# Kernel tuning notes

Measured on AMD Instinct MI355X. Metric: run time of the kernel, lower is better.

Reference implementation:

```python
import jax, jax.numpy as jnp
import numpy as np
from jax import lax

B, C, H, W = 32, 256, 56, 56

def _conv(x, w, stride, groups=1, pad='VALID'):
    return lax.conv_general_dilated(x, w, (stride, stride), pad,
                                    feature_group_count=groups,
                                    dimension_numbers=('NCHW', 'OIHW', 'NCHW'))

def _ln(x, g, b, eps=1e-5):
    mu = jnp.mean(x, -1, keepdims=True)
    var = jnp.mean((x - mu) ** 2, -1, keepdims=True)
    return (x - mu) * lax.rsqrt(var + eps) * g + b

def setup_inputs() -> dict:
    key = jax.random.key(0)
    ks = jax.random.split(key, 16)
    s = 0.02
    Ch = C // 2
    d = {}
    d['x'] = jax.random.normal(ks[0], (B, C, H, W), jnp.float32)
    d['Wq'] = jax.random.normal(ks[1], (C, C), jnp.float32) * s;  d['bq'] = jnp.zeros((C,), jnp.float32)
    d['Wk'] = jax.random.normal(ks[2], (C, C), jnp.float32) * s;  d['bk'] = jnp.zeros((C,), jnp.float32)
    d['Wv'] = jax.random.normal(ks[3], (C, C), jnp.float32) * s;  d['bv'] = jnp.zeros((C,), jnp.float32)
    d['sr1_w'] = jax.random.normal(ks[4], (C, C, 8, 8), jnp.float32) * s; d['sr1_b'] = jnp.zeros((C,), jnp.float32)
    d['ln1_g'] = jnp.ones((C,), jnp.float32); d['ln1_b'] = jnp.zeros((C,), jnp.float32)
    d['sr2_w'] = jax.random.normal(ks[5], (C, C, 4, 4), jnp.float32) * s; d['sr2_b'] = jnp.zeros((C,), jnp.float32)
    d['ln2_g'] = jnp.ones((C,), jnp.float32); d['ln2_b'] = jnp.zeros((C,), jnp.float32)
    d['Wkv1'] = jax.random.normal(ks[6], (C, C), jnp.float32) * s; d['bkv1'] = jnp.zeros((C,), jnp.float32)
    d['Wkv2'] = jax.random.normal(ks[7], (C, C), jnp.float32) * s; d['bkv2'] = jnp.zeros((C,), jnp.float32)
    d['lc1_w'] = jax.random.normal(ks[8], (Ch, 1, 3, 3), jnp.float32) * s; d['lc1_b'] = jnp.zeros((Ch,), jnp.float32)
    d['lc2_w'] = jax.random.normal(ks[9], (Ch, 1, 3, 3), jnp.float32) * s; d['lc2_b'] = jnp.zeros((Ch,), jnp.float32)
    d['rp_w'] = jax.random.normal(ks[10], (C, C), jnp.float32) * s;  d['rp_b'] = jnp.zeros((C,), jnp.float32)
    d['rp12_w'] = jax.random.normal(ks[11], (C, C), jnp.float32) * s; d['rp12_b'] = jnp.zeros((C,), jnp.float32)
    d['dw_w'] = jax.random.normal(ks[12], (C, 2), jnp.float32) * 0.5  # Conv3d (2,1,1) depthwise, no bias
    return d

def reference(x, Wq, bq, Wk, bk, Wv, bv, sr1_w, sr1_b, ln1_g, ln1_b,
              sr2_w, sr2_b, ln2_g, ln2_b, Wkv1, bkv1, Wkv2, bkv2,
              lc1_w, lc1_b, lc2_w, lc2_b, rp_w, rp_b, rp12_w, rp12_b, dw_w):
    Bx, Cc, h, w = x.shape
    N = h * w
    Ch = Cc // 2
    xt = x.reshape(Bx, Cc, N).transpose(0, 2, 1)                 # [B,N,C]
    q = jax.nn.softmax(xt @ Wq + bq, axis=-1)                    # softmax over channels
    q1, q2 = q[..., :Ch], q[..., Ch:]

    # spatial-reduction branches (conv -> LN -> GELU)
    x1 = _conv(x, sr1_w, 8) + sr1_b[:, None, None]               # [B,C,7,7]
    x1 = jax.nn.gelu(_ln(x1.reshape(Bx, Cc, -1).transpose(0, 2, 1), ln1_g, ln1_b), approximate=False)
    x2 = _conv(x, sr2_w, 4) + sr2_b[:, None, None]               # [B,C,14,14]
    x2 = jax.nn.gelu(_ln(x2.reshape(Bx, Cc, -1).transpose(0, 2, 1), ln2_g, ln2_b), approximate=False)

    def branch(xr, Wkv, bkv, lc_w, lc_b, qh, hh):
        kv = (xr @ Wkv + bkv).reshape(Bx, -1, 2, Ch)
        k = jax.nn.softmax(kv[:, :, 0], axis=1)                  # softmax over reduced tokens
        v = kv[:, :, 1]
        vsp = v.transpose(0, 2, 1).reshape(Bx, Ch, hh, hh)
        v = v + (_conv(vsp, lc_w, 1, groups=Ch, pad='SAME') + lc_b[:, None, None]).reshape(Bx, Ch, -1).transpose(0, 2, 1)
        ctx = jnp.einsum('bnk,bnv->bkv', k, v)                   # [B,Ch,Ch]
        return jnp.einsum('bnk,bkv->bnv', qh, ctx)               # [B,N,Ch]

    a1 = branch(x1, Wkv1, bkv1, lc1_w, lc1_b, q1, 7)
    a2 = branch(x2, Wkv2, bkv2, lc2_w, lc2_b, q2, 14)
    eff2 = jnp.concatenate([a1, a2], axis=-1)                    # [B,N,C]
    eff2 = jnp.einsum('bni,oi->bon', eff2, rp12_w).reshape(Bx, Cc, h, w) + rp12_b[None, :, None, None]

    # global efficient-attention branch
    keys = jax.nn.softmax(xt @ Wk + bk, axis=1)                  # softmax over tokens
    values = xt @ Wv + bv
    ctx = jnp.einsum('bnk,bnv->bkv', keys, values)               # [B,C,C]
    att = jnp.einsum('bnk,bkv->bnv', q, ctx)                     # [B,N,C]
    eff = jnp.einsum('bni,oi->bon', att, rp_w).reshape(Bx, Cc, h, w) + rp_b[None, :, None, None]

    # Conv3d (2,1,1) depthwise merge over the two branches
    out = eff * dw_w[:, 0][None, :, None, None] + eff2 * dw_w[:, 1][None, :, None, None]
    return out
```

## Files before the change

kernel.cpp:

```cpp
#include <hip/hip_runtime.h>
#include <hip/hip_bf16.h>
#include <math.h>

#define B_ 32
#define H_ 56
#define W_ 56
#define N_ 3136
#define NT_ 100352

typedef short short8 __attribute__((ext_vector_type(8)));
typedef float f32x4 __attribute__((ext_vector_type(4)));

__device__ __forceinline__ unsigned short f2b(float f){
  union { float f; unsigned u; } v; v.f = f;
  return (unsigned short)((v.u + 0x7FFFu + ((v.u>>16)&1u)) >> 16);
}

#define LDSW(row, bo) ((unsigned)((row)*128 + ((bo) ^ (((row)&7)<<4))))

__device__ __forceinline__ short8 ldfrag(const char* base, int row, int kk){
  return *(const short8*)(base + LDSW(row, kk*2));
}
__device__ __forceinline__ f32x4 mfma16(short8 a, short8 b, f32x4 c){
  return __builtin_amdgcn_mfma_f32_16x16x32_bf16(a, b, c, 0, 0, 0);
}
__device__ __forceinline__ void gld16(void* lds, const void* g){
  __builtin_amdgcn_global_load_lds((__attribute__((address_space(1))) void*)g,
                                   (__attribute__((address_space(3))) void*)lds,
                                   16, 0, 0);
}

__global__ void prep_trans_kernel(
    const float* __restrict__ x, unsigned short* __restrict__ xt,
    const float* __restrict__ Wq, const float* __restrict__ Wk,
    const float* __restrict__ Wv, const float* __restrict__ Wkv1,
    const float* __restrict__ Wkv2, const float* __restrict__ sr1w,
    const float* __restrict__ sr2w, const float* __restrict__ rpw,
    const float* __restrict__ rpb, const float* __restrict__ rp12w,
    const float* __restrict__ rp12b, const float* __restrict__ dww,
    unsigned short* WqT, unsigned short* WkT, unsigned short* WvT,
    unsigned short* Wkv1T, unsigned short* Wkv2T,
    unsigned short* srw1, unsigned short* srw2,
    unsigned short* Acomb, float* bias_out)
{
  __shared__ float tile[64][65];
  if (blockIdx.x < 6272){
    int bn = blockIdx.x >> 2; int b = bn / 49; int n0 = (bn - b*49)*64;
    int c0 = (blockIdx.x & 3)*64;
    int t = threadIdx.x;
    {
      int cl = t >> 2, nq = t & 3;
      const float* src = x + ((size_t)(b*256 + c0 + cl))*N_ + n0 + nq*16;
#pragma unroll
      for (int j = 0; j < 4; j++){
        float4 v = *(const float4*)(src + j*4);
        tile[cl][nq*16 + j*4 + 0] = v.x;
        tile[cl][nq*16 + j*4 + 1] = v.y;
        tile[cl][nq*16 + j*4 + 2] = v.z;
        tile[cl][nq*16 + j*4 + 3] = v.w;
      }
    }
    __syncthreads();
    {
      int nl = t >> 2, cq = t & 3;
      unsigned short pk[16];
#pragma unroll
      for (int j=0;j<16;j++) pk[j] = f2b(tile[cq*16+j][nl]);
      unsigned short* dst = xt + ((size_t)(b*N_ + n0 + nl))*256 + c0 + cq*16;
      *(uint4*)dst = *(uint4*)&pk[0];
      *(uint4*)(dst+8) = *(uint4*)&pk[8];
    }
    return;
  }
  int idx = (blockIdx.x - 6272)*256 + threadIdx.x;
  const int stride = 2048*256;
  const int total = 5*65536 + 4194304 + 1048576 + 131072 + 256;
  for (int i = idx; i < total; i += stride) {
    int j = i;
    if (j < 5*65536) {
      int w = j >> 16, e = j & 65535;
      int o = e >> 8, c = e & 255;
      const float* src = (w==0)?Wq:(w==1)?Wk:(w==2)?Wv:(w==3)?Wkv1:Wkv2;
      unsigned short* dst = (w==0)?WqT:(w==1)?WkT:(w==2)?WvT:(w==3)?Wkv1T:Wkv2T;
      dst[o*256+c] = f2b(src[c*256+o]);
      continue;
    }
    j -= 5*65536;
    if (j < 4194304) {
      int o = j >> 14, rem = j & 16383, pos = rem >> 8, c = rem & 255;
      srw1[j] = f2b(sr1w[o*16384 + c*64 + pos]);
      continue;
    }
    j -= 4194304;
    if (j < 1048576) {
      int o = j >> 12, rem = j & 4095, pos = rem >> 8, c = rem & 255;
      srw2[j] = f2b(sr2w[o*4096 + c*16 + pos]);
      continue;
    }
    j -= 1048576;
    if (j < 131072) {
      int o = j >> 9, i2 = j & 511;
      float v = (i2 < 256) ? dww[o*2+0]*rpw[o*256+i2]
                           : dww[o*2+1]*rp12w[o*256+(i2-256)];
      Acomb[o*512+i2] = f2b(v);
      continue;
    }
    j -= 131072;
    bias_out[j] = dww[j*2+0]*rpb[j] + dww[j*2+1]*rp12b[j];
  }
}

__global__ __launch_bounds__(256,2) void qkv3_kernel(
    const unsigned short* __restrict__ xt,
    const unsigned short* __restrict__ WqT, const unsigned short* __restrict__ WkT,
    const unsigned short* __restrict__ WvT,
    const float* __restrict__ bq, const float* __restrict__ bk, const float* __restrict__ bv,
    unsigned short* __restrict__ qbuf, unsigned short* __restrict__ KexpT,
    unsigned short* __restrict__ VT, float* __restrict__ s_q, float* __restrict__ s_k)
{
  __shared__ __align__(16) char smem[32768 + 32768 + 1024];
  char* At = smem;
  char* Bt = smem + 32768;
  float* redbuf = (float*)(smem + 65536);
  const int t = threadIdx.x, wave = t>>6, lane = t&63, l15 = lane&15, l4 = lane>>4;
  const int r0 = blockIdx.x*64;
  const int b = r0 / N_;
  const int nl0 = r0 - b*N_;

#pragma unroll
  for (int c4=0;c4<4;c4++)
#pragma unroll
    for (int j=0;j<2;j++){
      int chunk = j*256 + t; int row = chunk>>3, c8 = chunk&7;
      int c8s = c8 ^ (row&7);
      gld16(At + c4*8192 + (j*256 + wave*64)*16,
            xt + (size_t)(r0+row)*256 + c4*64 + c8s*8);
    }
  __syncthreads();

  for (int mat=0; mat<3; mat++){
    const unsigned short* BT = (mat==0)?WqT:(mat==1)?WkT:WvT;
    const float* bias = (mat==0)?bq:(mat==1)?bk:bv;
    const f32x4 vzero = {0.f,0.f,0.f,0.f};
    f32x4 acc[4][4];
#pragma unroll
    for (int i=0;i<4;i++)
#pragma unroll
      for (int j=0;j<4;j++) acc[i][j] = vzero;

    for (int k0c=0;k0c<4;k0c++){
#pragma unroll
      for (int j=0;j<8;j++){
        int chunk = j*256 + t; int row = chunk>>3, c8 = chunk&7;
        int c8s = c8 ^ (row&7);
        gld16(Bt + (j*256 + wave*64)*16, BT + (size_t)row*256 + k0c*64 + c8s*8);
      }
      __syncthreads();
#pragma unroll
      for (int ks=0;ks<2;ks++){
        short8 af[4], bfr[4];
#pragma unroll
        for (int mi=0;mi<4;mi++) af[mi]  = ldfrag(At + k0c*8192, mi*16 + l15, ks*32 + l4*8);
#pragma unroll
        for (int ni=0;ni<4;ni++) bfr[ni] = ldfrag(Bt, wave*64 + ni*16 + l15, ks*32 + l4*8);
#pragma unroll
        for (int mi=0;mi<4;mi++)
#pragma unroll
          for (int ni=0;ni<4;ni++)
            acc[mi][ni] = mfma16(af[mi], bfr[ni], acc[mi][ni]);
      }
      __syncthreads();
    }

    float bb4[4];
#pragma unroll
    for (int ni=0;ni<4;ni++) bb4[ni] = bias[wave*64 + ni*16 + l15];

    if (mat == 0) {
      float rs[4][4];
#pragma unroll
      for (int mi=0;mi<4;mi++)
#pragma unroll
        for (int r=0;r<4;r++) rs[mi][r] = 0.f;
#pragma unroll
      for (int mi=0;mi<4;mi++)
#pragma unroll
        for (int ni=0;ni<4;ni++)
#pragma unroll
          for (int r=0;r<4;r++){
            float e = __expf(acc[mi][ni][r] + bb4[ni]);
            acc[mi][ni][r] = e;
            rs[mi][r] += e;
          }
#pragma unroll
      for (int mi=0;mi<4;mi++)
#pragma unroll
        for (int r=0;r<4;r++){
          float s = rs[mi][r];
          s += __shfl_xor(s, 1); s += __shfl_xor(s, 2);
          s += __shfl_xor(s, 4); s += __shfl_xor(s, 8);
          rs[mi][r] = s;
        }
      if (l15 == 0){
#pragma unroll
        for (int mi=0;mi<4;mi++)
#pragma unroll
          for (int r=0;r<4;r++)
            redbuf[wave*64 + mi*16 + l4*4 + r] = rs[mi][r];
      }
      __syncthreads();
      unsigned short* qb = (unsigned short*)Bt;
#pragma unroll
      for (int mi=0;mi<4;mi++)
#pragma unroll
        for (int r=0;r<4;r++){
          int rr = mi*16 + l4*4 + r;
#pragma unroll
          for (int ni=0;ni<4;ni++)
            qb[rr*256 + wave*64 + ni*16 + l15] = f2b(acc[mi][ni][r]);
        }
      if (t < 64){
        s_q[r0 + t] = redbuf[t] + redbuf[64+t] + redbuf[128+t] + redbuf[192+t];
      }
      __syncthreads();
#pragma unroll
      for (int j=0;j<8;j++){
        int chunk = j*256 + t;
        int row = chunk >> 5, c8 = chunk & 31;
        *(uint4*)(qbuf + (size_t)(r0+row)*256 + c8*8) = *(const uint4*)(qb + row*256 + c8*8);
      }
      __syncthreads();
    } else {
      float cs[4] = {0.f,0.f,0.f,0.f};
#pragma unroll
      for (int mi=0;mi<4;mi++)
#pragma unroll
        for (int ni=0;ni<4;ni++)
#pragma unroll
          for (int r=0;r<4;r++){
            float v = acc[mi][ni][r] + bb4[ni];
            if (mat == 1){ v = __expf(v); cs[ni] += v; }
            int row = mi*16 + l4*4 + r;
            int col = wave*64 + ni*16 + l15;
            *(unsigned short*)(Bt + LDSW(col, row*2)) = f2b(v);
          }
      if (mat == 1){
#pragma unroll
        for (int ni=0;ni<4;ni++){
          float s = cs[ni];
          s += __shfl_xor(s, 16);
          s += __shfl_xor(s, 32);
          if (lane < 16) atomicAdd(&s_k[b*256 + wave*64 + ni*16 + lane], s);
        }
      }
      __syncthreads();
      unsigned short* ot = (mat==1) ? KexpT : VT;
#pragma unroll
      for (int j=0;j<8;j++){
        int chunk = j*256 + t;
        int c = chunk >> 3, n8 = chunk & 7;
        *(uint4*)(ot + ((size_t)b*256 + c)*N_ + nl0 + n8*8) = *(const uint4*)(Bt + LDSW(c, n8*16));
      }
      __syncthreads();
    }
  }
}

template<int S, int OW, int KW, int NSK, int MPB, int KTOT>
__device__ __forceinline__ void srconv_body(
    const unsigned short* __restrict__ xt, const unsigned short* __restrict__ wbf,
    float* __restrict__ part, int bid, char* At, char* Bt)
{
  const int KCH = KTOT / NSK;
  const int Mtot = B_*MPB;
  const int sk = bid % NSK, tile = bid / NSK;
  const int t = threadIdx.x, wave = t>>6, lane = t&63, l15 = lane&15, l4 = lane>>4;
  const f32x4 vzero = {0.f,0.f,0.f,0.f};
  f32x4 acc[4][4];
#pragma unroll
  for (int i=0;i<4;i++)
#pragma unroll
    for (int j=0;j<4;j++) acc[i][j] = vzero;

  size_t abase[2];
#pragma unroll
  for (int j=0;j<2;j++){
    int chunk = j*256 + t;
    int row = chunk >> 3, c8 = chunk & 7;
    int c8s = c8 ^ (row&7);
    int rowc = tile*64 + row; if (rowc > Mtot-1) rowc = Mtot-1;
    int b = rowc / MPB; int m = rowc - b*MPB;
    int p = m / OW; int q = m - p*OW;
    abase[j] = ((size_t)b*N_ + (size_t)(S*p)*W_ + S*q)*256 + c8s*8;
  }

  for (int kt = 0; kt < KCH; kt += 64){
    const int k0 = sk*KCH + kt;
    const int pos = k0 >> 8, cc = k0 & 255;
    const int dy = pos / KW, dx = pos - dy*KW;
    const size_t off = (size_t)(dy*W_ + dx)*256 + cc;
#pragma unroll
    for (int j=0;j<2;j++){
      gld16(At + (j*256 + wave*64)*16, xt + abase[j] + off);
    }
#pragma unroll
    for (int j=0;j<8;j++){
      int chunk = j*256 + t; int row = chunk>>3, c8 = chunk&7;
      int c8s = c8 ^ (row&7);
      gld16(Bt + (j*256 + wave*64)*16, wbf + (size_t)row*KTOT + k0 + c8s*8);
    }
    __syncthreads();
#pragma unroll
    for (int ks=0;ks<2;ks++){
      short8 af[4], bfr[4];
#pragma unroll
      for (int mi=0;mi<4;mi++) af[mi]  = ldfrag(At, mi*16 + l15, ks*32 + l4*8);
#pragma unroll
      for (int ni=0;ni<4;ni++) bfr[ni] = ldfrag(Bt, wave*64 + ni*16 + l15, ks*32 + l4*8);
#pragma unroll
      for (int mi=0;mi<4;mi++)
#pragma unroll
        for (int ni=0;ni<4;ni++)
          acc[mi][ni] = mfma16(af[mi], bfr[ni], acc[mi][ni]);
    }
    __syncthreads();
  }
#pragma unroll
  for (int mi=0;mi<4;mi++)
#pragma unroll
    for (int r=0;r<4;r++){
      int row = tile*64 + mi*16 + l4*4 + r;
      if (row < Mtot){
        size_t basep = ((size_t)sk*Mtot + row)*256;
#pragma unroll
        for (int ni=0;ni<4;ni++)
          part[basep + wave*64 + ni*16 + l15] = acc[mi][ni][r];
      }
    }
}

__device__ __forceinline__ void ctxmain_body(
    const unsigned short* __restrict__ KexpT, const unsigned short* __restrict__ VT,
    float* __restrict__ part, int orig, char* At, char* Bt)
{
  const int idx = (orig & 7)*112 + (orig >> 3);
  const int b = idx / 28; int rem = idx - b*28;
  const int sk = rem >> 2, y = rem & 3;
  const int mt = y >> 1, nt = y & 1;
  const int it0 = sk*7, it1 = it0+7;
  const int t = threadIdx.x;
  const int wave = t>>6, lane = t&63, l15 = lane&15, l4 = lane>>4;
  const int wm = (wave>>1)*64, wn = (wave&1)*64;
  const unsigned short* A  = KexpT + ((size_t)b*256 + mt*128)*N_;
  const unsigned short* Bv = VT + ((size_t)b*256 + nt*128)*N_;
  const f32x4 vzero = {0.f,0.f,0.f,0.f};
  f32x4 acc[4][4];
#pragma unroll
  for (int i=0;i<4;i++)
#pragma unroll
    for (int j=0;j<4;j++) acc[i][j] = vzero;

  for (int it=it0; it<it1; it++){
    const int k0 = it*64;
#pragma unroll
    for (int j=0;j<4;j++){
      int chunk = j*256 + t; int row = chunk>>3, c8 = chunk&7;
      int c8s = c8 ^ (row&7);
      gld16(At + (j*256 + wave*64)*16, A + (size_t)row*N_ + k0 + c8s*8);
    }
#pragma unroll
    for (int j=0;j<4;j++){
      int chunk = j*256 + t; int row = chunk>>3, c8 = chunk&7;
      int c8s = c8 ^ (row&7);
      gld16(Bt + (j*256 + wave*64)*16, Bv + (size_t)row*N_ + k0 + c8s*8);
    }
    __syncthreads();
#pragma unroll
    for (int ks=0;ks<2;ks++){
      short8 af[4], bfr[4];
#pragma unroll
      for (int mi=0;mi<4;mi++) af[mi]  = ldfrag(At, wm + mi*16 + l15, ks*32 + l4*8);
#pragma unroll
      for (int ni=0;ni<4;ni++) bfr[ni] = ldfrag(Bt, wn + ni*16 + l15, ks*32 + l4*8);
#pragma unroll
      for (int mi=0;mi<4;mi++)
#pragma unroll
        for (int ni=0;ni<4;ni++)
          acc[mi][ni] = mfma16(af[mi], bfr[ni], acc[mi][ni]);
    }
    __syncthreads();
  }
#pragma unroll
  for (int mi=0;mi<4;mi++)
#pragma unroll
    for (int r=0;r<4;r++){
      int kg = mt*128 + wm + mi*16 + l4*4 + r;
      size_t basep = (((size_t)sk*B_ + b)*256 + kg)*256 + nt*128 + wn;
#pragma unroll
      for (int ni=0;ni<4;ni++)
        part[basep + ni*16 + l15] = acc[mi][ni][r];
    }
}

__global__ __launch_bounds__(256,4) void conv_ctx_kernel(
    const unsigned short* __restrict__ xt, const unsigned short* __restrict__ srw1,
    const unsigned short* __restrict__ srw2, float* __restrict__ x1part,
    float* __restrict__ x2part, const unsigned short* __restrict__ KexpT,
    const unsigned short* __restrict__ VT, float* __restrict__ ctxpart)
{
  __shared__ __align__(16) char smem[8192 + 32768];
  if (blockIdx.x < 392)
    srconv_body<4,14,4,4,196,4096>(xt, srw2, x2part, blockIdx.x, smem, smem+8192);
  else if (blockIdx.x < 792)
    srconv_body<8,7,8,16,49,16384>(xt, srw1, x1part, blockIdx.x-392, smem, smem+8192);
  else
    ctxmain_body(KexpT, VT, ctxpart, blockIdx.x-792, smem, smem+16384);
}

__device__ __forceinline__ void lngelu_body(
    const float* __restrict__ part, const float* __restrict__ srb,
    const float* __restrict__ g, const float* __restrict__ bb,
    unsigned short* __restrict__ out, int M, int nsk, int Mtot, int bid,
    float* red)
{
  int b = bid / M, m = bid - b*M;
  int c = threadIdx.x;
  float v = srb[c];
  for (int s=0;s<nsk;s++) v += part[((size_t)s*Mtot + b*M + m)*256 + c];
  int wave = c>>6, lane = c&63;
  float s1 = v;
  s1 += __shfl_xor(s1,1); s1 += __shfl_xor(s1,2); s1 += __shfl_xor(s1,4);
  s1 += __shfl_xor(s1,8); s1 += __shfl_xor(s1,16); s1 += __shfl_xor(s1,32);
  if (lane==0) red[wave] = s1;
  __syncthreads();
  float mu = (red[0]+red[1]+red[2]+red[3]) * (1.0f/256.0f);
  float d = v - mu;
  float s2 = d*d;
  s2 += __shfl_xor(s2,1); s2 += __shfl_xor(s2,2); s2 += __shfl_xor(s2,4);
  s2 += __shfl_xor(s2,8); s2 += __shfl_xor(s2,16); s2 += __shfl_xor(s2,32);
  if (lane==0) red[4+wave] = s2;
  __syncthreads();
  float var = (red[4]+red[5]+red[6]+red[7]) * (1.0f/256.0f);
  float y = d * rsqrtf(var + 1e-5f) * g[c] + bb[c];
  float ge = 0.5f * y * (1.0f + erff(y * 0.70710678118654752f));
  out[((size_t)b*M + m)*256 + c] = f2b(ge);
}

__global__ __launch_bounds__(256) void red_ln_kernel(
    const float* __restrict__ x1part, const float* __restrict__ x2part,
    const float* __restrict__ sr1b, const float* __restrict__ sr2b,
    const float* __restrict__ ln1g, const float* __restrict__ ln1b,
    const float* __restrict__ ln2g, const float* __restrict__ ln2b,
    unsigned short* __restrict__ x1g, unsigned short* __restrict__ x2g,
    const float* __restrict__ ctxpart, const float* __restrict__ s_k,
    unsigned short* __restrict__ ctxcomb)
{
  __shared__ float red[8];
  if (blockIdx.x < 1568){
    lngelu_body(x1part, sr1b, ln1g, ln1b, x1g, 49, 16, 1568, blockIdx.x, red);
  } else if (blockIdx.x < 7840){
    lngelu_body(x2part, sr2b, ln2g, ln2b, x2g, 196, 4, 6272, blockIdx.x-1568, red);
  } else {
    int e = ((blockIdx.x-7840)*256 + threadIdx.x)*4;
    int b = e >> 16; int rem = e & 65535; int kg = rem >> 8; int col = rem & 255;
    float4 s = {0.f,0.f,0.f,0.f};
#pragma unroll
    for (int sk=0; sk<7; sk++){
      float4 p = *(const float4*)(ctxpart + ((((size_t)sk*B_ + b)*256 + kg)<<8) + col);
      s.x += p.x; s.y += p.y; s.z += p.z; s.w += p.w;
    }
    float inv = 1.0f / s_k[b*256 + kg];
    unsigned short pk[4] = {f2b(s.x*inv), f2b(s.y*inv), f2b(s.z*inv), f2b(s.w*inv)};
    *(uint2*)(ctxcomb + ((size_t)b*256 + kg)*512 + col) = *(uint2*)&pk[0];
  }
}

__global__ __launch_bounds__(256,2) void gmat_kernel(
    const unsigned short* __restrict__ Acomb, const unsigned short* __restrict__ ctxcomb,
    unsigned short* __restrict__ outg)
{
  __shared__ __align__(16) char smem[32768];
  char* At = smem; char* Bt = smem + 16384;
  const int b = blockIdx.x, mt = blockIdx.y, nt = blockIdx.z;
  const int t = threadIdx.x;
  const int wave = t>>6, lane = t&63, l15 = lane&15, l4 = lane>>4;
  const int wm = (wave>>1)*64, wn = (wave&1)*64;
  const unsigned short* A  = Acomb + (size_t)mt*128*512;
  const unsigned short* Bv = ctxcomb + ((size_t)b*256 + nt*128)*512;
  const f32x4 vzero = {0.f,0.f,0.f,0.f};
  f32x4 acc[4][4];
#pragma unroll
  for (int i=0;i<4;i++)
#pragma unroll
    for (int j=0;j<4;j++) acc[i][j] = vzero;

  for (int it=0; it<8; it++){
    const int k0 = it*64;
#pragma unroll
    for (int j=0;j<4;j++){
      int chunk = j*256 + t; int row = chunk>>3, c8 = chunk&7;
      int c8s = c8 ^ (row&7);
      gld16(At + (j*256 + wave*64)*16, A + (size_t)row*512 + k0 + c8s*8);
    }
#pragma unroll
    for (int j=0;j<4;j++){
      int chunk = j*256 + t; int row = chunk>>3, c8 = chunk&7;
      int c8s = c8 ^ (row&7);
      gld16(Bt + (j*256 + wave*64)*16, Bv + (size_t)row*512 + k0 + c8s*8);
    }
    __syncthreads();
#pragma unroll
    for (int ks=0;ks<2;ks++){
      short8 af[4], bfr[4];
#pragma unroll
      for (int mi=0;mi<4;mi++) af[mi]  = ldfrag(At, wm + mi*16 + l15, ks*32 + l4*8);
#pragma unroll
      for (int ni=0;ni<4;ni++) bfr[ni] = ldfrag(Bt, wn + ni*16 + l15, ks*32 + l4*8);
#pragma unroll
      for (int mi=0;mi<4;mi++)
#pragma unroll
        for (int ni=0;ni<4;ni++)
          acc[mi][ni] = mfma16(af[mi], bfr[ni], acc[mi][ni]);
    }
    __syncthreads();
  }
#pragma unroll
  for (int mi=0;mi<4;mi++)
#pragma unroll
    for (int r=0;r<4;r++){
      int og = mt*128 + wm + mi*16 + l4*4 + r;
#pragma unroll
      for (int ni=0;ni<4;ni++)
        outg[(size_t)b*65536 + (size_t)og*256 + nt*128 + wn + ni*16 + l15] = f2b(acc[mi][ni][r]);
    }
}

__global__ __launch_bounds__(256,4) void kv_both_kernel(
    const unsigned short* __restrict__ x1g, const unsigned short* __restrict__ Wkv1T,
    const float* __restrict__ bkv1, float* __restrict__ kexp1, float* __restrict__ vraw1,
    const unsigned short* __restrict__ x2g, const unsigned short* __restrict__ Wkv2T,
    const float* __restrict__ bkv2, float* __restrict__ kexp2, float* __restrict__ vraw2)
{
  __shared__ __align__(16) char smem[8192 + 16384];
  char* At = smem; char* Bt = smem + 8192;
  const int half = blockIdx.x & 1;
  int bid = blockIdx.x >> 1;
  const unsigned short* A; const unsigned short* BT; const float* bias;
  float* kexp; float* vraw; int r0; int R;
  if (bid < 25){ A=x1g; BT=Wkv1T; bias=bkv1; kexp=kexp1; vraw=vraw1; r0=bid*64; R=1568; }
  else { A=x2g; BT=Wkv2T; bias=bkv2; kexp=kexp2; vraw=vraw2; r0=(bid-25)*64; R=6272; }
  const int t = threadIdx.x, wave = t>>6, lane = t&63, l15 = lane&15, l4 = lane>>4;
  const int wn = wave*32;
  const f32x4 vzero = {0.f,0.f,0.f,0.f};
  f32x4 acc[4][2];
#pragma unroll
  for (int i=0;i<4;i++){ acc[i][0] = vzero; acc[i][1] = vzero; }

  for (int k0 = 0; k0 < 256; k0 += 64) {
#pragma unroll
    for (int j = 0; j < 2; j++){
      int chunk = j*256 + t;
      int row = chunk >> 3, c8 = chunk & 7;
      int c8s = c8 ^ (row&7);
      int rg = r0 + row; if (rg > R-1) rg = R-1;
      gld16(At + (j*256 + wave*64)*16, A + (size_t)rg*256 + k0 + c8s*8);
    }
#pragma unroll
    for (int j = 0; j < 4; j++){
      int chunk = j*256 + t;
      int row = chunk >> 3, c8 = chunk & 7;
      int c8s = c8 ^ (row&7);
      gld16(Bt + (j*256 + wave*64)*16, BT + (size_t)(half*128 + row)*256 + k0 + c8s*8);
    }
    __syncthreads();
#pragma unroll
    for (int ks = 0; ks < 2; ks++){
      short8 af[4], bfr[2];
#pragma unroll
      for (int mi=0;mi<4;mi++) af[mi]  = ldfrag(At, mi*16 + l15, ks*32 + l4*8);
#pragma unroll
      for (int ni=0;ni<2;ni++) bfr[ni] = ldfrag(Bt, wn + ni*16 + l15, ks*32 + l4*8);
#pragma unroll
      for (int mi=0;mi<4;mi++)
#pragma unroll
        for (int ni=0;ni<2;ni++)
          acc[mi][ni] = mfma16(af[mi], bfr[ni], acc[mi][ni]);
    }
    __syncthreads();
  }
  float bb2[2];
#pragma unroll
  for (int ni=0;ni<2;ni++) bb2[ni] = bias[half*128 + wn + ni*16 + l15];
#pragma unroll
  for (int mi=0;mi<4;mi++)
#pragma unroll
    for (int ni=0;ni<2;ni++)
#pragma unroll
      for (int r=0;r<4;r++){
        int rg = r0 + mi*16 + l4*4 + r;
        if (rg < R){
          int col = wn + ni*16 + l15;
          float v = acc[mi][ni][r] + bb2[ni];
          if (half == 0) kexp[(size_t)rg*128 + col] = __expf(v);
          else           vraw[(size_t)rg*128 + col] = v;
        }
      }
}

__device__ __forceinline__ void dwconv_body(
    const float* __restrict__ vraw, const float* __restrict__ lcw,
    const float* __restrict__ lcb, float* __restrict__ vmod, int M, int OW, int idx)
{
  int ch = idx & 127; int rest = idx >> 7; int m = rest % M; int b = rest / M;
  if (b >= B_) return;
  int py = m / OW, px = m - py*OW;
  float acc = vraw[((size_t)b*M + m)*128 + ch] + lcb[ch];
#pragma unroll
  for (int dy=0;dy<3;dy++)
#pragma unroll
    for (int dx=0;dx<3;dx++){
      int yy = py+dy-1, xx = px+dx-1;
      if (yy>=0 && yy<OW && xx>=0 && xx<OW)
        acc += vraw[((size_t)b*M + yy*OW+xx)*128 + ch] * lcw[ch*9 + dy*3 + dx];
    }
  vmod[((size_t)b*M + m)*128 + ch] = acc;
}

__global__ __launch_bounds__(256) void dwconv_both_kernel(
    const float* __restrict__ vraw1, const float* __restrict__ lc1w,
    const float* __restrict__ lc1b, float* __restrict__ vmod1,
    const float* __restrict__ vraw2, const float* __restrict__ lc2w,
    const float* __restrict__ lc2b, float* __restrict__ vmod2)
{
  int gid = blockIdx.x*256 + threadIdx.x;
  if (blockIdx.x < 784) dwconv_body(vraw1, lc1w, lc1b, vmod1, 49, 7, gid);
  else dwconv_body(vraw2, lc2w, lc2b, vmod2, 196, 14, gid - 784*256);
}

__global__ __launch_bounds__(512) void ctxbr_both_kernel(
    const float* __restrict__ kexp1, const float* __restrict__ vmod1,
    const float* __restrict__ kexp2, const float* __restrict__ vmod2,
    unsigned short* __restrict__ ctxcomb)
{
  const int b = blockIdx.x;
  int kc = blockIdx.y;
  const float* kexp; const float* vmod; int M, BR;
  if (kc < 32){ kexp = kexp1; vmod = vmod1; M = 49; BR = 0; }
  else { kexp = kexp2; vmod = vmod2; M = 196; BR = 1; kc -= 32; }
  const int t = threadIdx.x;
  const int kl = t >> 7, j = t & 127;
  const int kk = kc*4 + kl;
  const float* kp = kexp + (size_t)b*M*128 + kk;
  const float* vp = vmod + (size_t)b*M*128 + j;
  float acc = 0.f, s = 0.f;
  for (int m = 0; m < M; m++){
    float kv = kp[(size_t)m*128];
    s += kv;
    acc += kv * vp[(size_t)m*128];
  }
  const int krow = BR ? (128+kk) : kk;
  unsigned short* dst = ctxcomb + ((size_t)b*256 + krow)*512;
  const int wbase = BR ? 384 : 256;
  const int zbase = BR ? 256 : 384;
  dst[wbase + j] = f2b(acc / s);
  dst[zbase + j] = 0;
}

__global__ __launch_bounds__(256,4) void final_kernel(
    const unsigned short* __restrict__ Gmat, const unsigned short* __restrict__ qbuf,
    const float* __restrict__ bias_out, const float* __restrict__ s_q,
    float* __restrict__ out)
{
  __shared__ __align__(16) char smem[16384 + 8192];
  char* At = smem; char* Bt = smem + 16384;
  const int b = blockIdx.x, ot = blockIdx.y, nt = blockIdx.z;
  const int t = threadIdx.x, wave = t>>6, lane = t&63, l15 = lane&15, l4 = lane>>4;
  const int wm = (wave>>1)*64, wn = (wave&1)*32;
  const unsigned short* A  = Gmat + ((size_t)b*256 + ot*128)*256;
  const unsigned short* Bq = qbuf + ((size_t)b*N_ + nt*64)*256;
  const f32x4 vzero = {0.f,0.f,0.f,0.f};
  f32x4 acc[4][2];
#pragma unroll
  for (int i=0;i<4;i++){ acc[i][0] = vzero; acc[i][1] = vzero; }

  for (int k0=0;k0<256;k0+=64){
#pragma unroll
    for (int j=0;j<4;j++){
      int chunk = j*256 + t; int row = chunk>>3, c8 = chunk&7;
      int c8s = c8 ^ (row&7);
      gld16(At + (j*256 + wave*64)*16, A + (size_t)row*256 + k0 + c8s*8);
    }
#pragma unroll
    for (int j=0;j<2;j++){
      int chunk = j*256 + t; int row = chunk>>3, c8 = chunk&7;
      int c8s = c8 ^ (row&7);
      gld16(Bt + (j*256 + wave*64)*16, Bq + (size_t)row*256 + k0 + c8s*8);
    }
    __syncthreads();
#pragma unroll
    for (int ks=0;ks<2;ks++){
      short8 af[4], bfr[2];
#pragma unroll
      for (int mi=0;mi<4;mi++) af[mi]  = ldfrag(At, wm + mi*16 + l15, ks*32 + l4*8);
#pragma unroll
      for (int ni=0;ni<2;ni++) bfr[ni] = ldfrag(Bt, wn + ni*16 + l15, ks*32 + l4*8);
#pragma unroll
      for (int mi=0;mi<4;mi++)
#pragma unroll
        for (int ni=0;ni<2;ni++)
          acc[mi][ni] = mfma16(af[mi], bfr[ni], acc[mi][ni]);
    }
    __syncthreads();
  }
  float iq[2];
#pragma unroll
  for (int ni=0;ni<2;ni++)
    iq[ni] = 1.0f / s_q[(size_t)b*N_ + nt*64 + wn + ni*16 + l15];
#pragma unroll
  for (int mi=0;mi<4;mi++)
#pragma unroll
    for (int r=0;r<4;r++){
      int o = ot*128 + wm + mi*16 + l4*4 + r;
      float bo = bias_out[o];
#pragma unroll
      for (int ni=0;ni<2;ni++){
        int n = nt*64 + wn + ni*16 + l15;
        out[((size_t)b*256 + o)*N_ + n] = acc[mi][ni][r]*iq[ni] + bo;
      }
    }
}

extern "C" void kernel_launch(void* const* d_in, const int* in_sizes, int n_in,
                              void* d_out, int out_size, void* d_ws, size_t ws_size,
                              hipStream_t stream)
{
  const float* x     = (const float*)d_in[0];
  const float* Wq    = (const float*)d_in[1];
  const float* bq    = (const float*)d_in[2];
  const float* Wk    = (const float*)d_in[3];
  const float* bk    = (const float*)d_in[4];
  const float* Wv    = (const float*)d_in[5];
  const float* bv    = (const float*)d_in[6];
  const float* sr1w  = (const float*)d_in[7];
  const float* sr1b  = (const float*)d_in[8];
  const float* ln1g  = (const float*)d_in[9];
  const float* ln1b  = (const float*)d_in[10];
  const float* sr2w  = (const float*)d_in[11];
  const float* sr2b  = (const float*)d_in[12];
  const float* ln2g  = (const float*)d_in[13];
  const float* ln2b  = (const float*)d_in[14];
  const float* Wkv1  = (const float*)d_in[15];
  const float* bkv1  = (const float*)d_in[16];
  const float* Wkv2  = (const float*)d_in[17];
  const float* bkv2  = (const float*)d_in[18];
  const float* lc1w  = (const float*)d_in[19];
  const float* lc1b  = (const float*)d_in[20];
  const float* lc2w  = (const float*)d_in[21];
  const float* lc2b  = (const float*)d_in[22];
  const float* rpw   = (const float*)d_in[23];
  const float* rpb   = (const float*)d_in[24];
  const float* rp12w = (const float*)d_in[25];
  const float* rp12b = (const float*)d_in[26];
  const float* dww   = (const float*)d_in[27];

  char* ws = (char*)d_ws;
  size_t off = 0;
  auto take = [&](size_t n)->char*{ char* p = ws + off; off += (n + 255) & ~(size_t)255; return p; };

  unsigned short* WqT   = (unsigned short*)take(131072);
  unsigned short* WkT   = (unsigned short*)take(131072);
  unsigned short* WvT   = (unsigned short*)take(131072);
  unsigned short* Wkv1T = (unsigned short*)take(131072);
  unsigned short* Wkv2T = (unsigned short*)take(131072);
  unsigned short* srw1  = (unsigned short*)take(8388608);
  unsigned short* srw2  = (unsigned short*)take(2097152);
  unsigned short* Acomb = (unsigned short*)take(262144);
  float* bias_out = (float*)take(1024);
  float* s_k      = (float*)take(32768);
  float* s_q      = (float*)take(401408);
  char* regionA = take(51380224);
  unsigned short* qbuf = (unsigned short*)take(51380224);
  char* regionK = take(51380224);
  char* regionV = take(51380224);
  float* x1part = (float*)take(25690112);
  if (off > ws_size) return;

  unsigned short* xt    = (unsigned short*)regionA;
  unsigned short* KexpT = (unsigned short*)regionK;
  unsigned short* VT = (unsigned short*)regionV;
  unsigned short* Gmat = (unsigned short*)regionV;
  unsigned short* x1g  = (unsigned short*)(regionV + 4194304);
  unsigned short* x2g  = (unsigned short*)(regionV + 4997120);
  float* kexp1 = (float*)(regionV + 8208384);
  float* vraw1 = (float*)(regionV + 9011200);
  float* vmod1 = (float*)(regionV + 9814016);
  float* kexp2 = (float*)(regionV + 10616832);
  float* vraw2 = (float*)(regionV + 13828096);
  float* vmod2 = (float*)(regionV + 17039360);
  unsigned short* ctxcomb = (unsigned short*)d_out;
  float* ctxpart = (float*)((char*)d_out + 8388608);
  float* x2part  = (float*)((char*)d_out + 67108864);

  hipMemsetAsync(s_k, 0, 32768, stream);
  prep_trans_kernel<<<8320, 256, 0, stream>>>(x, xt,
                                              Wq, Wk, Wv, Wkv1, Wkv2, sr1w, sr2w,
                                              rpw, rpb, rp12w, rp12b, dww,
                                              WqT, WkT, WvT, Wkv1T, Wkv2T, srw1, srw2,
                                              Acomb, bias_out);
  qkv3_kernel<<<1568, 256, 0, stream>>>(xt, WqT, WkT, WvT, bq, bk, bv,
                                        qbuf, KexpT, VT, s_q, s_k);
  conv_ctx_kernel<<<392+400+896, 256, 0, stream>>>(xt, srw1, srw2,
                                                   x1part, x2part, KexpT, VT, ctxpart);
  red_ln_kernel<<<7840+2048, 256, 0, stream>>>(x1part, x2part, sr1b, sr2b,
                                               ln1g, ln1b, ln2g, ln2b, x1g, x2g,
                                               ctxpart, s_k, ctxcomb);
  kv_both_kernel<<<246, 256, 0, stream>>>(x1g, Wkv1T, bkv1, kexp1, vraw1,
                                          x2g, Wkv2T, bkv2, kexp2, vraw2);
  dwconv_both_kernel<<<3920, 256, 0, stream>>>(vraw1, lc1w, lc1b, vmod1,
                                               vraw2, lc2w, lc2b, vmod2);
  ctxbr_both_kernel<<<dim3(32,64), 512, 0, stream>>>(kexp1, vmod1, kexp2, vmod2, ctxcomb);
  gmat_kernel<<<dim3(32,2,2), 256, 0, stream>>>(Acomb, ctxcomb, Gmat);
  final_kernel<<<dim3(32,2,49), 256, 0, stream>>>(Gmat, qbuf, bias_out, s_q, (float*)d_out);
}
```

Measured before the change: 400.9 us.

## Co-schedule spatial-reduction convs with QKV projection and split out context GEMM

The strided spatial-reduction convolutions move out of the context kernel and into the QKV projection launch, interleaved two QKV blocks to one conv block by block index. The context GEMM becomes its own kernel. Both convs and the QKV GEMM read only xt, so they can overlap on the GPU instead of the convs waiting for QKV to finish. The trade-offs are that the conv blocks now run under the QKV kernel's larger shared-memory footprint and 256x2 launch bounds, which may lower their occupancy, and that the separate context kernel adds one launch.

```diff
diff --git a/kernel.cpp b/kernel.cpp
--- a/kernel.cpp
+++ b/kernel.cpp
@@ -110,20 +110,20 @@
   }
 }
 
-__global__ __launch_bounds__(256,2) void qkv3_kernel(
+__device__ __forceinline__ void qkv3_body(
     const unsigned short* __restrict__ xt,
     const unsigned short* __restrict__ WqT, const unsigned short* __restrict__ WkT,
     const unsigned short* __restrict__ WvT,
     const float* __restrict__ bq, const float* __restrict__ bk, const float* __restrict__ bv,
     unsigned short* __restrict__ qbuf, unsigned short* __restrict__ KexpT,
-    unsigned short* __restrict__ VT, float* __restrict__ s_q, float* __restrict__ s_k)
-{
-  __shared__ __align__(16) char smem[32768 + 32768 + 1024];
+    unsigned short* __restrict__ VT, float* __restrict__ s_q, float* __restrict__ s_k,
+    int blkid, char* smem)
+{
   char* At = smem;
   char* Bt = smem + 32768;
   float* redbuf = (float*)(smem + 65536);
   const int t = threadIdx.x, wave = t>>6, lane = t&63, l15 = lane&15, l4 = lane>>4;
-  const int r0 = blockIdx.x*64;
+  const int r0 = blkid*64;
   const int b = r0 / N_;
   const int nl0 = r0 - b*N_;
 
@@ -339,10 +339,37 @@
     }
 }
 
-__device__ __forceinline__ void ctxmain_body(
+__global__ __launch_bounds__(256,2) void qkv_conv_kernel(
+    const unsigned short* __restrict__ xt,
+    const unsigned short* __restrict__ WqT, const unsigned short* __restrict__ WkT,
+    const unsigned short* __restrict__ WvT,
+    const float* __restrict__ bq, const float* __restrict__ bk, const float* __restrict__ bv,
+    unsigned short* __restrict__ qbuf, unsigned short* __restrict__ KexpT,
+    unsigned short* __restrict__ VT, float* __restrict__ s_q, float* __restrict__ s_k,
+    const unsigned short* __restrict__ srw1, const unsigned short* __restrict__ srw2,
+    float* __restrict__ x1part, float* __restrict__ x2part)
+{
+  __shared__ __align__(16) char smem[32768 + 32768 + 1024];
+  const int r = blockIdx.x % 3, q = blockIdx.x / 3;
+  if (r < 2){
+    int qk = 2*q + r;
+    if (qk >= 1568) return;
+    qkv3_body(xt, WqT, WkT, WvT, bq, bk, bv, qbuf, KexpT, VT, s_q, s_k, qk, smem);
+  } else {
+    if (q < 392)
+      srconv_body<4,14,4,4,196,4096>(xt, srw2, x2part, q, smem, smem+8192);
+    else
+      srconv_body<8,7,8,16,49,16384>(xt, srw1, x1part, q-392, smem, smem+8192);
+  }
+}
+
+__global__ __launch_bounds__(256,4) void ctxmain_kernel(
     const unsigned short* __restrict__ KexpT, const unsigned short* __restrict__ VT,
-    float* __restrict__ part, int orig, char* At, char* Bt)
-{
+    float* __restrict__ part)
+{
+  __shared__ __align__(16) char smem[32768];
+  char* At = smem; char* Bt = smem + 16384;
+  const int orig = blockIdx.x;
   const int idx = (orig & 7)*112 + (orig >> 3);
   const int b = idx / 28; int rem = idx - b*28;
   const int sk = rem >> 2, y = rem & 3;
@@ -400,21 +427,6 @@
       for (int ni=0;ni<4;ni++)
         part[basep + ni*16 + l15] = acc[mi][ni][r];
     }
-}
-
-__global__ __launch_bounds__(256,4) void conv_ctx_kernel(
-    const unsigned short* __restrict__ xt, const unsigned short* __restrict__ srw1,
-    const unsigned short* __restrict__ srw2, float* __restrict__ x1part,
-    float* __restrict__ x2part, const unsigned short* __restrict__ KexpT,
-    const unsigned short* __restrict__ VT, float* __restrict__ ctxpart)
-{
-  __shared__ __align__(16) char smem[8192 + 32768];
-  if (blockIdx.x < 392)
-    srconv_body<4,14,4,4,196,4096>(xt, srw2, x2part, blockIdx.x, smem, smem+8192);
-  else if (blockIdx.x < 792)
-    srconv_body<8,7,8,16,49,16384>(xt, srw1, x1part, blockIdx.x-392, smem, smem+8192);
-  else
-    ctxmain_body(KexpT, VT, ctxpart, blockIdx.x-792, smem, smem+16384);
 }
 
 __device__ __forceinline__ void lngelu_body(
@@ -807,10 +819,10 @@
                                               rpw, rpb, rp12w, rp12b, dww,
                                               WqT, WkT, WvT, Wkv1T, Wkv2T, srw1, srw2,
                                               Acomb, bias_out);
-  qkv3_kernel<<<1568, 256, 0, stream>>>(xt, WqT, WkT, WvT, bq, bk, bv,
-                                        qbuf, KexpT, VT, s_q, s_k);
-  conv_ctx_kernel<<<392+400+896, 256, 0, stream>>>(xt, srw1, srw2,
-                                                   x1part, x2part, KexpT, VT, ctxpart);
+  qkv_conv_kernel<<<2376, 256, 0, stream>>>(xt, WqT, WkT, WvT, bq, bk, bv,
+                                            qbuf, KexpT, VT, s_q, s_k,
+                                            srw1, srw2, x1part, x2part);
+  ctxmain_kernel<<<896, 256, 0, stream>>>(KexpT, VT, ctxpart);
   red_ln_kernel<<<7840+2048, 256, 0, stream>>>(x1part, x2part, sr1b, sr2b,
                                                ln1g, ln1b, ln2g, ln2b, x1g, x2g,
                                                ctxpart, s_k, ctxcomb);
```

Measured after the change: 407.8 us. About the same (+1.7%).
